# Optimization experiments

Hardware: AMD Instinct MI355X
Metric: run time of the kernel (lower is better)

Reference implementation:

```python
import jax, jax.numpy as jnp
import numpy as np

N_NODES = 50000
N_EDGES = 800000
D = 64          # node_in_feats == out_feats
N_STEPS = 3


def setup_inputs() -> dict:
    key = jax.random.key(0)
    ks = jax.random.split(key, 9)
    s = 1.0 / np.sqrt(D)
    return {
        "node_in": jax.random.normal(ks[0], (N_NODES, D), jnp.float32),
        # edge-type-0 linear (DGL GatedGraphConv self.linears[0])
        "W": jax.random.uniform(ks[1], (D, D), jnp.float32, -s, s),
        "b": jax.random.uniform(ks[2], (D,), jnp.float32, -s, s),
        # GRUCell params (torch layout: rows = [r, z, n] blocks)
        "Wih": jax.random.uniform(ks[3], (3 * D, D), jnp.float32, -s, s),
        "Whh": jax.random.uniform(ks[4], (3 * D, D), jnp.float32, -s, s),
        "bih": jax.random.uniform(ks[5], (3 * D,), jnp.float32, -s, s),
        "bhh": jax.random.uniform(ks[6], (3 * D,), jnp.float32, -s, s),
        "src": jax.random.randint(ks[7], (N_EDGES,), 0, N_NODES, jnp.int32),
        "dst": jax.random.randint(ks[8], (N_EDGES,), 0, N_NODES, jnp.int32),
    }


def _gru_cell(x, h, Wih, Whh, bih, bhh):
    gi = x @ Wih.T + bih   # [N, 3D]
    gh = h @ Whh.T + bhh   # [N, 3D]
    i_r, i_z, i_n = jnp.split(gi, 3, axis=-1)
    h_r, h_z, h_n = jnp.split(gh, 3, axis=-1)
    r = jax.nn.sigmoid(i_r + h_r)
    z = jax.nn.sigmoid(i_z + h_z)
    n = jnp.tanh(i_n + r * h_n)
    return (1.0 - z) * n + z * h


def reference(node_in, W, b, Wih, Whh, bih, bhh, src, dst):
    # DGL GatedGraphConv, n_steps=3, n_etypes=1. node_in_feats == out_feats,
    # so no zero-padding needed. The wrapper's tanh/dropout result is
    # discarded (h is overwritten by the second conv1 call), so the module
    # output is exactly one GatedGraphConv forward.
    h = node_in
    for _ in range(N_STEPS):
        wh = h @ W.T + b                                   # per-node transform; edge msg = wh[src]
        msg = wh[src]                                      # [E, D] gather
        a = jax.ops.segment_sum(msg, dst, num_segments=N_NODES)  # scatter-sum aggregation
        h = _gru_cell(a, h, Wih, Whh, bih, bhh)
    return h
```

## Files before the change

### kernel.cpp

```cpp
#include <hip/hip_runtime.h>

#define D 64
#define EXS 388
#define SGS 72
#define CHUNK 8192
#define PTH 512
#define MAXB 4096

typedef __bf16 bf16x8 __attribute__((ext_vector_type(8)));
typedef float f32x4 __attribute__((ext_vector_type(4)));

union U16 { uint4 u; bf16x8 b; };

__device__ __forceinline__ unsigned short f2bf(float f) {
    unsigned u = __float_as_uint(f);
    u += 0x7fff + ((u >> 16) & 1);
    return (unsigned short)(u >> 16);
}
__device__ __forceinline__ float bf2f(unsigned short s) {
    return __uint_as_float(((unsigned)s) << 16);
}


__global__ __launch_bounds__(256) void phist_kernel(const int* __restrict__ dst,
                                                    int* __restrict__ hist2,
                                                    int E, int G, int NBUK) {
    __shared__ int h[512];
    int g = blockIdx.x;
    for (int i = threadIdx.x; i < NBUK; i += 256) h[i] = 0;
    __syncthreads();
    int beg = g * CHUNK;
    int end = min(beg + CHUNK, E);
    for (int i = beg + threadIdx.x; i < end; i += 256)
        atomicAdd(&h[dst[i] >> 7], 1);
    __syncthreads();
    for (int i = threadIdx.x; i < NBUK; i += 256)
        hist2[i * G + g] = h[i];
}

__global__ __launch_bounds__(256) void gsum_kernel(const int* __restrict__ a,
                                                   int* __restrict__ bsums, int n) {
    int base = blockIdx.x * 1024 + threadIdx.x * 4;
    int s = 0;
    if (base + 3 < n) {
        int4 v = *(const int4*)(a + base);
        s = v.x + v.y + v.z + v.w;
    } else {
        for (int j = 0; j < 4; ++j) if (base + j < n) s += a[base + j];
    }
    for (int st = 1; st < 64; st <<= 1) s += __shfl_xor(s, st, 64);
    __shared__ int wsum[4];
    if ((threadIdx.x & 63) == 0) wsum[threadIdx.x >> 6] = s;
    __syncthreads();
    if (threadIdx.x == 0) bsums[blockIdx.x] = wsum[0] + wsum[1] + wsum[2] + wsum[3];
}

__global__ __launch_bounds__(64) void gbscan_kernel(int* __restrict__ bsums, int nb) {
    int l = threadIdx.x;
    int own = (l < nb) ? bsums[l] : 0;
    int v = own;
    for (int st = 1; st < 64; st <<= 1) {
        int t = __shfl_up(v, st, 64);
        if (l >= st) v += t;
    }
    if (l < nb) bsums[l] = v - own;
}

__global__ __launch_bounds__(256) void gscan_kernel(int* __restrict__ a,
                                                    const int* __restrict__ bsums, int n) {
    int tid = threadIdx.x;
    int base = blockIdx.x * 1024 + tid * 4;
    int c0 = 0, c1 = 0, c2 = 0, c3 = 0;
    if (base + 3 < n) {
        int4 v = *(const int4*)(a + base);
        c0 = v.x; c1 = v.y; c2 = v.z; c3 = v.w;
    } else {
        if (base < n) c0 = a[base];
        if (base + 1 < n) c1 = a[base + 1];
        if (base + 2 < n) c2 = a[base + 2];
    }
    int s = c0 + c1 + c2 + c3;
    int l = tid & 63, w = tid >> 6;
    int v = s;
    for (int st = 1; st < 64; st <<= 1) {
        int t = __shfl_up(v, st, 64);
        if (l >= st) v += t;
    }
    __shared__ int wsum[4];
    if (l == 63) wsum[w] = v;
    __syncthreads();
    int woff = 0;
    for (int j = 0; j < w; ++j) woff += wsum[j];
    int excl = bsums[blockIdx.x] + woff + (v - s);
    int4 o;
    o.x = excl; o.y = excl + c0; o.z = excl + c0 + c1; o.w = excl + c0 + c1 + c2;
    if (base + 3 < n) {
        *(int4*)(a + base) = o;
    } else {
        int t[4] = {o.x, o.y, o.z, o.w};
        for (int j = 0; j < 4; ++j) if (base + j < n) a[base + j] = t[j];
    }
}

__global__ __launch_bounds__(PTH) void partition_kernel(const int* __restrict__ src,
                                                        const int* __restrict__ dst,
                                                        const int* __restrict__ off2,
                                                        unsigned* __restrict__ pairs,
                                                        int E, int G, int NBUK) {
    __shared__ unsigned pl[CHUNK];
    __shared__ unsigned short bk[CHUNK];
    __shared__ int hist[512];
    __shared__ int scn[512];
    __shared__ int goff[512];
    int g = blockIdx.x;
    int t = threadIdx.x;
    int beg = g * CHUNK;
    int end = min(beg + CHUNK, E);
    int m = end - beg;
    hist[t] = 0;
    __syncthreads();
    for (int i = t; i < m; i += PTH)
        atomicAdd(&hist[dst[beg + i] >> 7], 1);
    __syncthreads();
    int own = hist[t];
    scn[t] = own;
    __syncthreads();
    for (int off = 1; off < 512; off <<= 1) {
        int cur = scn[t];
        int add = (t >= off) ? scn[t - off] : 0;
        __syncthreads();
        scn[t] = cur + add;
        __syncthreads();
    }
    int excl = scn[t] - own;
    hist[t] = excl;
    if (t < NBUK) goff[t] = off2[t * G + g] - excl;
    __syncthreads();
    for (int i = t; i < m; i += PTH) {
        int d = dst[beg + i];
        int s = src[beg + i];
        int b = d >> 7;
        int pos = atomicAdd(&hist[b], 1);
        pl[pos] = ((unsigned)s << 7) | (unsigned)(d & 127);
        bk[pos] = (unsigned short)b;
    }
    __syncthreads();
    for (int i = t; i < m; i += PTH)
        pairs[goff[bk[i]] + i] = pl[i];
}

__global__ __launch_bounds__(256) void bucket_sort_kernel(const unsigned* __restrict__ pairs,
                                                          const int* __restrict__ off2,
                                                          int* __restrict__ srcs_sorted,
                                                          int* __restrict__ row_off,
                                                          int E, int G, int NBUK, int N) {
    __shared__ unsigned pl[MAXB];
    __shared__ int srcl[MAXB];
    __shared__ int cnt[128];
    __shared__ int sc[128];
    __shared__ int cur2[128];
    int b = blockIdx.x;
    int t = threadIdx.x;
    int beg = off2[b * G];
    int end = (b == NBUK - 1) ? E : off2[(b + 1) * G];
    int m = end - beg;
    if (m > MAXB) m = MAXB;
    if (t < 128) cnt[t] = 0;
    __syncthreads();
    for (int i = t; i < m; i += 256) {
        unsigned p = pairs[beg + i];
        pl[i] = p;
        atomicAdd(&cnt[p & 127], 1);
    }
    __syncthreads();
    int vt = 0;
    if (t < 128) { vt = cnt[t]; sc[t] = vt; }
    __syncthreads();
    for (int off = 1; off < 128; off <<= 1) {
        int v2 = 0;
        if (t < 128) { v2 = sc[t] + ((t >= off) ? sc[t - off] : 0); }
        __syncthreads();
        if (t < 128) sc[t] = v2;
        __syncthreads();
    }
    int excl = (t < 128) ? (sc[t] - vt) : 0;
    if (t < 128) {
        int gid = b * 128 + t;
        if (gid < N) row_off[gid] = beg + excl;
        cur2[t] = excl;
    }
    if (b == NBUK - 1 && t == 0) row_off[N] = E;
    __syncthreads();
    for (int i = t; i < m; i += 256) {
        unsigned p = pl[i];
        int r = atomicAdd(&cur2[p & 127], 1);
        srcl[r] = (int)(p >> 7);
    }
    __syncthreads();
    for (int i = t; i < m; i += 256) srcs_sorted[beg + i] = srcl[i];
}


__global__ __launch_bounds__(128) void pack_b_kernel(const float* __restrict__ W,
                                                     const float* __restrict__ Wih,
                                                     const float* __restrict__ Whh,
                                                     const float* __restrict__ b,
                                                     unsigned short* __restrict__ Bpack,
                                                     float* __restrict__ cvec) {
    int blk = blockIdx.x;
    int g = blk >> 2, t = blk & 3;
    int ks = threadIdx.x >> 6, lane = threadIdx.x & 63;
    int col = (g % 3) * 64 + t * 16 + (lane & 15);
    int kbase = ks * 32 + ((lane >> 4) & 3) * 8;
    size_t base = ((size_t)(blk * 2 + ks) * 64 + lane) * 8;
#pragma unroll
    for (int j = 0; j < 8; ++j) {
        int k = kbase + j;
        float v;
        if (g < 3) {
            v = 0.f;
#pragma unroll
            for (int m = 0; m < D; ++m) v += Wih[col * D + m] * W[m * D + k];
        } else {
            v = Whh[col * D + k];
        }
        Bpack[base + j] = f2bf(v);
    }
    if (g < 3 && ks == 0 && ((lane >> 4) & 3) == 0) {
        float acc = 0.f;
#pragma unroll
        for (int k = 0; k < D; ++k) acc += Wih[col * D + k] * b[k];
        cvec[col] = acc;
    }
}

__global__ void cvt_kernel(const float* __restrict__ in, unsigned short* __restrict__ out0,
                           unsigned short* __restrict__ out1, int n4, int N) {
    int i = blockIdx.x * 256 + threadIdx.x;
    if (i < n4) {
        float4 v = ((const float4*)in)[i];
        ushort4 o;
        o.x = f2bf(v.x); o.y = f2bf(v.y); o.z = f2bf(v.z); o.w = f2bf(v.w);
        ((ushort4*)out0)[i] = o;
    }
    if (blockIdx.x == 0 && threadIdx.x < 16) {
        ((ushort4*)(out0 + (size_t)N * D))[threadIdx.x] = (ushort4){0, 0, 0, 0};
        ((ushort4*)(out1 + (size_t)N * D))[threadIdx.x] = (ushort4){0, 0, 0, 0};
    }
}


__global__ __launch_bounds__(512) void fused2_kernel(const unsigned short* __restrict__ hb_in,
                                                     unsigned short* __restrict__ hb_out,
                                                     float* __restrict__ Fout, int writeF32,
                                                     const unsigned short* __restrict__ Bpack,
                                                     const float* __restrict__ cvec,
                                                     const float* __restrict__ bih,
                                                     const float* __restrict__ bhh,
                                                     const int* __restrict__ row_off,
                                                     const int* __restrict__ srcs,
                                                     int N) {
    __shared__ unsigned short sg[16 * SGS];
    __shared__ float ex[16 * EXS];
    int tid = threadIdx.x;
    int g = tid >> 6;
    int lane = tid & 63;
    int base = blockIdx.x * 16;

    {
        int es = lane >> 3;
        int fo = lane & 7;
        int nlA = g, nlB = g + 8;
        int nodeA = base + nlA, nodeB = base + nlB;
        int begA = 0, endA = 0, begB = 0, endB = 0;
        if (nodeA < N) { begA = row_off[nodeA]; endA = row_off[nodeA + 1]; }
        if (nodeB < N) { begB = row_off[nodeB]; endB = row_off[nodeB + 1]; }

        int sA[4], sB[4];
#pragma unroll
        for (int j = 0; j < 4; ++j) {
            int eA = begA + 8 * j + es;
            int eB = begB + 8 * j + es;
            sA[j] = (eA < endA) ? srcs[eA] : N;
            sB[j] = (eB < endB) ? srcs[eB] : N;
        }
        uint4 dA[4], dB[4];
#pragma unroll
        for (int j = 0; j < 4; ++j) dA[j] = *(const uint4*)(hb_in + (size_t)sA[j] * D + fo * 8);
#pragma unroll
        for (int j = 0; j < 4; ++j) dB[j] = *(const uint4*)(hb_in + (size_t)sB[j] * D + fo * 8);

        float accA[8], accB[8];
#pragma unroll
        for (int j = 0; j < 8; ++j) { accA[j] = 0.f; accB[j] = 0.f; }
#pragma unroll
        for (int j = 0; j < 4; ++j) {
            unsigned ua[4] = {dA[j].x, dA[j].y, dA[j].z, dA[j].w};
            unsigned ub[4] = {dB[j].x, dB[j].y, dB[j].z, dB[j].w};
#pragma unroll
            for (int k = 0; k < 4; ++k) {
                accA[2 * k]     += bf2f((unsigned short)(ua[k] & 0xffff));
                accA[2 * k + 1] += bf2f((unsigned short)(ua[k] >> 16));
                accB[2 * k]     += bf2f((unsigned short)(ub[k] & 0xffff));
                accB[2 * k + 1] += bf2f((unsigned short)(ub[k] >> 16));
            }
        }
        for (int i = begA + 32; i < endA; i += 8) {
            int e = i + es;
            int s = (e < endA) ? srcs[e] : N;
            uint4 dd = *(const uint4*)(hb_in + (size_t)s * D + fo * 8);
            unsigned uu[4] = {dd.x, dd.y, dd.z, dd.w};
#pragma unroll
            for (int k = 0; k < 4; ++k) {
                accA[2 * k]     += bf2f((unsigned short)(uu[k] & 0xffff));
                accA[2 * k + 1] += bf2f((unsigned short)(uu[k] >> 16));
            }
        }
        for (int i = begB + 32; i < endB; i += 8) {
            int e = i + es;
            int s = (e < endB) ? srcs[e] : N;
            uint4 dd = *(const uint4*)(hb_in + (size_t)s * D + fo * 8);
            unsigned uu[4] = {dd.x, dd.y, dd.z, dd.w};
#pragma unroll
            for (int k = 0; k < 4; ++k) {
                accB[2 * k]     += bf2f((unsigned short)(uu[k] & 0xffff));
                accB[2 * k + 1] += bf2f((unsigned short)(uu[k] >> 16));
            }
        }
#pragma unroll
        for (int st = 8; st < 64; st <<= 1)
#pragma unroll
            for (int j = 0; j < 8; ++j) {
                accA[j] += __shfl_xor(accA[j], st, 64);
                accB[j] += __shfl_xor(accB[j], st, 64);
            }
        if (es == 0) {
            uint4 oA, oB;
            oA.x = (unsigned)f2bf(accA[0]) | ((unsigned)f2bf(accA[1]) << 16);
            oA.y = (unsigned)f2bf(accA[2]) | ((unsigned)f2bf(accA[3]) << 16);
            oA.z = (unsigned)f2bf(accA[4]) | ((unsigned)f2bf(accA[5]) << 16);
            oA.w = (unsigned)f2bf(accA[6]) | ((unsigned)f2bf(accA[7]) << 16);
            oB.x = (unsigned)f2bf(accB[0]) | ((unsigned)f2bf(accB[1]) << 16);
            oB.y = (unsigned)f2bf(accB[2]) | ((unsigned)f2bf(accB[3]) << 16);
            oB.z = (unsigned)f2bf(accB[4]) | ((unsigned)f2bf(accB[5]) << 16);
            oB.w = (unsigned)f2bf(accB[6]) | ((unsigned)f2bf(accB[7]) << 16);
            *(uint4*)(sg + nlA * SGS + fo * 8) = oA;
            *(uint4*)(sg + nlB * SGS + fo * 8) = oB;
        }
    }
    __syncthreads();

    if (g < 6) {
        int r16 = lane & 15, quad = lane >> 4;
        bf16x8 bf[4][2];
        const uint4* bp = (const uint4*)Bpack;
#pragma unroll
        for (int t = 0; t < 4; ++t)
#pragma unroll
            for (int ks = 0; ks < 2; ++ks) {
                U16 u; u.u = bp[((g * 4 + t) * 2 + ks) * 64 + lane];
                bf[t][ks] = u.b;
            }
        bf16x8 af[2];
        if (g < 3) {
#pragma unroll
            for (int ks = 0; ks < 2; ++ks) {
                U16 u; u.u = *(const uint4*)(sg + r16 * SGS + ks * 32 + quad * 8);
                af[ks] = u.b;
            }
        } else {
            int row = base + r16;
            if (row >= N) row = N - 1;
#pragma unroll
            for (int ks = 0; ks < 2; ++ks) {
                U16 u; u.u = *(const uint4*)(hb_in + (size_t)row * D + ks * 32 + quad * 8);
                af[ks] = u.b;
            }
        }
        f32x4 acc[4];
#pragma unroll
        for (int t = 0; t < 4; ++t) acc[t] = (f32x4){0.f, 0.f, 0.f, 0.f};
#pragma unroll
        for (int t = 0; t < 4; ++t)
#pragma unroll
            for (int ks = 0; ks < 2; ++ks)
                acc[t] = __builtin_amdgcn_mfma_f32_16x16x32_bf16(af[ks], bf[t][ks], acc[t], 0, 0, 0);
#pragma unroll
        for (int t = 0; t < 4; ++t)
#pragma unroll
            for (int r = 0; r < 4; ++r)
                ex[(quad * 4 + r) * EXS + g * 64 + t * 16 + r16] = acc[t][r];
    }
    __syncthreads();

    for (int idx = tid; idx < 16 * D; idx += 512) {
        int i = idx >> 6, d = idx & 63;
        int node = base + i;
        if (node < N) {
            const float* p = &ex[i * EXS];
            float deg = (float)(row_off[node + 1] - row_off[node]);
            float ir = p[d] + bih[d] + deg * cvec[d];
            float iz = p[64 + d] + bih[64 + d] + deg * cvec[64 + d];
            float in_ = p[128 + d] + bih[128 + d] + deg * cvec[128 + d];
            float hr = p[192 + d] + bhh[d];
            float hz = p[256 + d] + bhh[64 + d];
            float hn = p[320 + d] + bhh[128 + d];
            float h = bf2f(hb_in[(size_t)node * D + d]);
            float r = 1.f / (1.f + __expf(-(ir + hr)));
            float z = 1.f / (1.f + __expf(-(iz + hz)));
            float nn = tanhf(in_ + r * hn);
            float hnew = (1.f - z) * nn + z * h;
            hb_out[(size_t)node * D + d] = f2bf(hnew);
            if (writeF32) Fout[(size_t)node * D + d] = hnew;
        }
    }
}

extern "C" void kernel_launch(void* const* d_in, const int* in_sizes, int n_in,
                              void* d_out, int out_size, void* d_ws, size_t ws_size,
                              hipStream_t stream) {
    const float* node_in = (const float*)d_in[0];
    const float* W       = (const float*)d_in[1];
    const float* b       = (const float*)d_in[2];
    const float* Wih     = (const float*)d_in[3];
    const float* Whh     = (const float*)d_in[4];
    const float* bih     = (const float*)d_in[5];
    const float* bhh     = (const float*)d_in[6];
    const int*   src     = (const int*)d_in[7];
    const int*   dst     = (const int*)d_in[8];
    const int N = in_sizes[0] / D;
    const int E = in_sizes[7];
    float* out = (float*)d_out;

    const int G = (E + CHUNK - 1) / CHUNK;
    const int NBUK = (N + 127) >> 7;
    const int NSC = NBUK * G;
    const int NBLK = (NSC + 1023) / 1024;

    char* ws = (char*)d_ws;
    size_t off = 0;
    auto alloc = [&](size_t bytes) -> void* {
        void* p = ws + off;
        off += (bytes + 255) & ~(size_t)255;
        return p;
    };
    unsigned short* hb0    = (unsigned short*)alloc((size_t)(N + 1) * D * 2);
    unsigned short* hb1    = (unsigned short*)alloc((size_t)(N + 1) * D * 2);
    int*   row_off         = (int*)alloc((size_t)(N + 1) * sizeof(int));
    int*   srcs_sorted     = (int*)alloc((size_t)E * sizeof(int));
    unsigned* pairs        = (unsigned*)alloc((size_t)E * sizeof(unsigned));
    int*   hist2           = (int*)alloc((size_t)NSC * sizeof(int));
    int*   bsums           = (int*)alloc((size_t)NBLK * sizeof(int));
    unsigned short* Bpack  = (unsigned short*)alloc((size_t)6 * 4 * 2 * 64 * 8 * 2);
    float* cvec            = (float*)alloc((size_t)192 * sizeof(float));

    pack_b_kernel<<<24, 128, 0, stream>>>(W, Wih, Whh, b, Bpack, cvec);
    cvt_kernel<<<(N * D / 4 + 255) / 256, 256, 0, stream>>>(node_in, hb0, hb1, N * D / 4, N);

    phist_kernel<<<G, 256, 0, stream>>>(dst, hist2, E, G, NBUK);
    gsum_kernel<<<NBLK, 256, 0, stream>>>(hist2, bsums, NSC);
    gbscan_kernel<<<1, 64, 0, stream>>>(bsums, NBLK);
    gscan_kernel<<<NBLK, 256, 0, stream>>>(hist2, bsums, NSC);
    partition_kernel<<<G, PTH, 0, stream>>>(src, dst, hist2, pairs, E, G, NBUK);
    bucket_sort_kernel<<<NBUK, 256, 0, stream>>>(pairs, hist2, srcs_sorted, row_off,
                                                 E, G, NBUK, N);

    const int grid = (N + 15) / 16;
    fused2_kernel<<<grid, 512, 0, stream>>>(hb0, hb1, out, 0, Bpack, cvec, bih, bhh,
                                            row_off, srcs_sorted, N);
    fused2_kernel<<<grid, 512, 0, stream>>>(hb1, hb0, out, 0, Bpack, cvec, bih, bhh,
                                            row_off, srcs_sorted, N);
    fused2_kernel<<<grid, 512, 0, stream>>>(hb0, hb1, out, 1, Bpack, cvec, bih, bhh,
                                            row_off, srcs_sorted, N);
}
```

Before: 225.2 us.

## Replace per-chunk histogram scan with global bucket counts and atomic cursors

Replaces the bucket-by-chunk histogram with its three-kernel multi-block scan by global per-bucket counts accumulated with atomics, a single-block scan, and atomic cursor reservation in the partition kernel. This removes two kernel launches and the scan traffic over the NBUK×G array. In exchange, edges within a bucket are no longer laid out in a deterministic chunk order, and a memset is added. The later per-bucket sort keeps the final CSR correct, but the order of edges within a row, and so the float summation order, may vary between runs.

Result: no change. 227.1 us (+0.8%).

```diff
diff --git a/kernel.cpp b/kernel.cpp
--- a/kernel.cpp
+++ b/kernel.cpp
@@ -22,9 +22,9 @@
 }
 
 
-__global__ __launch_bounds__(256) void phist_kernel(const int* __restrict__ dst,
-                                                    int* __restrict__ hist2,
-                                                    int E, int G, int NBUK) {
+__global__ __launch_bounds__(256) void count_kernel(const int* __restrict__ dst,
+                                                    int* __restrict__ gcnt,
+                                                    int E, int NBUK) {
     __shared__ int h[512];
     int g = blockIdx.x;
     for (int i = threadIdx.x; i < NBUK; i += 256) h[i] = 0;
@@ -35,78 +35,38 @@
         atomicAdd(&h[dst[i] >> 7], 1);
     __syncthreads();
     for (int i = threadIdx.x; i < NBUK; i += 256)
-        hist2[i * G + g] = h[i];
-}
-
-__global__ __launch_bounds__(256) void gsum_kernel(const int* __restrict__ a,
-                                                   int* __restrict__ bsums, int n) {
-    int base = blockIdx.x * 1024 + threadIdx.x * 4;
-    int s = 0;
-    if (base + 3 < n) {
-        int4 v = *(const int4*)(a + base);
-        s = v.x + v.y + v.z + v.w;
-    } else {
-        for (int j = 0; j < 4; ++j) if (base + j < n) s += a[base + j];
-    }
-    for (int st = 1; st < 64; st <<= 1) s += __shfl_xor(s, st, 64);
-    __shared__ int wsum[4];
-    if ((threadIdx.x & 63) == 0) wsum[threadIdx.x >> 6] = s;
-    __syncthreads();
-    if (threadIdx.x == 0) bsums[blockIdx.x] = wsum[0] + wsum[1] + wsum[2] + wsum[3];
-}
-
-__global__ __launch_bounds__(64) void gbscan_kernel(int* __restrict__ bsums, int nb) {
-    int l = threadIdx.x;
-    int own = (l < nb) ? bsums[l] : 0;
-    int v = own;
-    for (int st = 1; st < 64; st <<= 1) {
-        int t = __shfl_up(v, st, 64);
-        if (l >= st) v += t;
-    }
-    if (l < nb) bsums[l] = v - own;
-}
-
-__global__ __launch_bounds__(256) void gscan_kernel(int* __restrict__ a,
-                                                    const int* __restrict__ bsums, int n) {
-    int tid = threadIdx.x;
-    int base = blockIdx.x * 1024 + tid * 4;
-    int c0 = 0, c1 = 0, c2 = 0, c3 = 0;
-    if (base + 3 < n) {
-        int4 v = *(const int4*)(a + base);
-        c0 = v.x; c1 = v.y; c2 = v.z; c3 = v.w;
-    } else {
-        if (base < n) c0 = a[base];
-        if (base + 1 < n) c1 = a[base + 1];
-        if (base + 2 < n) c2 = a[base + 2];
-    }
-    int s = c0 + c1 + c2 + c3;
-    int l = tid & 63, w = tid >> 6;
-    int v = s;
-    for (int st = 1; st < 64; st <<= 1) {
-        int t = __shfl_up(v, st, 64);
-        if (l >= st) v += t;
-    }
-    __shared__ int wsum[4];
-    if (l == 63) wsum[w] = v;
-    __syncthreads();
-    int woff = 0;
-    for (int j = 0; j < w; ++j) woff += wsum[j];
-    int excl = bsums[blockIdx.x] + woff + (v - s);
-    int4 o;
-    o.x = excl; o.y = excl + c0; o.z = excl + c0 + c1; o.w = excl + c0 + c1 + c2;
-    if (base + 3 < n) {
-        *(int4*)(a + base) = o;
-    } else {
-        int t[4] = {o.x, o.y, o.z, o.w};
-        for (int j = 0; j < 4; ++j) if (base + j < n) a[base + j] = t[j];
-    }
+        if (h[i]) atomicAdd(&gcnt[i], h[i]);
+}
+
+__global__ __launch_bounds__(512) void bscan_kernel(const int* __restrict__ gcnt,
+                                                    int* __restrict__ bucket_off,
+                                                    int* __restrict__ gcursor,
+                                                    int NBUK, int E) {
+    __shared__ int scn[512];
+    int t = threadIdx.x;
+    int own = (t < NBUK) ? gcnt[t] : 0;
+    scn[t] = own;
+    __syncthreads();
+    for (int off = 1; off < 512; off <<= 1) {
+        int cur = scn[t];
+        int add = (t >= off) ? scn[t - off] : 0;
+        __syncthreads();
+        scn[t] = cur + add;
+        __syncthreads();
+    }
+    if (t < NBUK) {
+        int excl = scn[t] - own;
+        bucket_off[t] = excl;
+        gcursor[t] = excl;
+    }
+    if (t == 0) bucket_off[NBUK] = E;
 }
 
 __global__ __launch_bounds__(PTH) void partition_kernel(const int* __restrict__ src,
                                                         const int* __restrict__ dst,
-                                                        const int* __restrict__ off2,
+                                                        int* __restrict__ gcursor,
                                                         unsigned* __restrict__ pairs,
-                                                        int E, int G, int NBUK) {
+                                                        int E, int NBUK) {
     __shared__ unsigned pl[CHUNK];
     __shared__ unsigned short bk[CHUNK];
     __shared__ int hist[512];
@@ -134,7 +94,10 @@
     }
     int excl = scn[t] - own;
     hist[t] = excl;
-    if (t < NBUK) goff[t] = off2[t * G + g] - excl;
+    if (t < NBUK) {
+        int gbase = own ? atomicAdd(&gcursor[t], own) : 0;
+        goff[t] = gbase - excl;
+    }
     __syncthreads();
     for (int i = t; i < m; i += PTH) {
         int d = dst[beg + i];
@@ -150,10 +113,10 @@
 }
 
 __global__ __launch_bounds__(256) void bucket_sort_kernel(const unsigned* __restrict__ pairs,
-                                                          const int* __restrict__ off2,
+                                                          const int* __restrict__ bucket_off,
                                                           int* __restrict__ srcs_sorted,
                                                           int* __restrict__ row_off,
-                                                          int E, int G, int NBUK, int N) {
+                                                          int E, int NBUK, int N) {
     __shared__ unsigned pl[MAXB];
     __shared__ int srcl[MAXB];
     __shared__ int cnt[128];
@@ -161,8 +124,8 @@
     __shared__ int cur2[128];
     int b = blockIdx.x;
     int t = threadIdx.x;
-    int beg = off2[b * G];
-    int end = (b == NBUK - 1) ? E : off2[(b + 1) * G];
+    int beg = bucket_off[b];
+    int end = bucket_off[b + 1];
     int m = end - beg;
     if (m > MAXB) m = MAXB;
     if (t < 128) cnt[t] = 0;
@@ -434,8 +397,6 @@
 
     const int G = (E + CHUNK - 1) / CHUNK;
     const int NBUK = (N + 127) >> 7;
-    const int NSC = NBUK * G;
-    const int NBLK = (NSC + 1023) / 1024;
 
     char* ws = (char*)d_ws;
     size_t off = 0;
@@ -449,21 +410,21 @@
     int*   row_off         = (int*)alloc((size_t)(N + 1) * sizeof(int));
     int*   srcs_sorted     = (int*)alloc((size_t)E * sizeof(int));
     unsigned* pairs        = (unsigned*)alloc((size_t)E * sizeof(unsigned));
-    int*   hist2           = (int*)alloc((size_t)NSC * sizeof(int));
-    int*   bsums           = (int*)alloc((size_t)NBLK * sizeof(int));
+    int*   gcnt            = (int*)alloc((size_t)NBUK * sizeof(int));
+    int*   bucket_off      = (int*)alloc((size_t)(NBUK + 1) * sizeof(int));
+    int*   gcursor         = (int*)alloc((size_t)NBUK * sizeof(int));
     unsigned short* Bpack  = (unsigned short*)alloc((size_t)6 * 4 * 2 * 64 * 8 * 2);
     float* cvec            = (float*)alloc((size_t)192 * sizeof(float));
 
     pack_b_kernel<<<24, 128, 0, stream>>>(W, Wih, Whh, b, Bpack, cvec);
     cvt_kernel<<<(N * D / 4 + 255) / 256, 256, 0, stream>>>(node_in, hb0, hb1, N * D / 4, N);
 
-    phist_kernel<<<G, 256, 0, stream>>>(dst, hist2, E, G, NBUK);
-    gsum_kernel<<<NBLK, 256, 0, stream>>>(hist2, bsums, NSC);
-    gbscan_kernel<<<1, 64, 0, stream>>>(bsums, NBLK);
-    gscan_kernel<<<NBLK, 256, 0, stream>>>(hist2, bsums, NSC);
-    partition_kernel<<<G, PTH, 0, stream>>>(src, dst, hist2, pairs, E, G, NBUK);
-    bucket_sort_kernel<<<NBUK, 256, 0, stream>>>(pairs, hist2, srcs_sorted, row_off,
-                                                 E, G, NBUK, N);
+    hipMemsetAsync(gcnt, 0, (size_t)NBUK * sizeof(int), stream);
+    count_kernel<<<G, 256, 0, stream>>>(dst, gcnt, E, NBUK);
+    bscan_kernel<<<1, 512, 0, stream>>>(gcnt, bucket_off, gcursor, NBUK, E);
+    partition_kernel<<<G, PTH, 0, stream>>>(src, dst, gcursor, pairs, E, NBUK);
+    bucket_sort_kernel<<<NBUK, 256, 0, stream>>>(pairs, bucket_off, srcs_sorted, row_off,
+                                                 E, NBUK, N);
 
     const int grid = (N + 15) / 16;
     fused2_kernel<<<grid, 512, 0, stream>>>(hb0, hb1, out, 0, Bpack, cvec, bih, bhh,
```
